# Kernel optimization log

Hardware: AMD Instinct MI355X
Metric: run time of the kernel (lower is better)

## Reference

```python
import jax, jax.numpy as jnp
import numpy as np

B, N, D = 4, 2048, 256
ALPHA = 0.2  # LeakyReLU negative slope
NEG = -1e9


def setup_inputs() -> dict:
    key = jax.random.key(0)
    ks = jax.random.split(key, 16)
    f = lambda k, s: jax.random.normal(k, s, dtype=jnp.float32)
    sc = 0.02
    spk = jax.random.randint(ks[13], (B, N), 0, 2)
    intra_mask = (spk[:, :, None] == spk[:, None, :]).astype(jnp.int32)
    inter_mask = 1 - intra_mask
    return {
        'inp': f(ks[0], (B, N, D)),
        'emo_vector': f(ks[1], (B, N, D)),
        'event_csk_before': f(ks[2], (B, N, D)),
        'event_csk_after': f(ks[3], (B, N, D)),
        'emo_intra_csk': f(ks[4], (B, N, D)),
        'emo_inter_csk': f(ks[5], (B, N, D)),
        'int_intra_csk': f(ks[6], (B, N, D)),
        'int_inter_csk': f(ks[7], (B, N, D)),
        'W': f(ks[8], (D, D)) * sc,
        'a': f(ks[9], (2 * D,)) * sc,
        'csk_W': f(ks[10], (D, D)) * sc,
        'csk_b': jnp.zeros((D,), jnp.float32),
        'emo_lin_W': f(ks[11], (4, D, D)) * sc,  # order: weight, query, key, value
        'emo_lin_b': jnp.zeros((4, D), jnp.float32),
        'act_lin_W': f(ks[12], (4, D, D)) * sc,
        'act_lin_b': jnp.zeros((4, D), jnp.float32),
        'conv_len': jax.random.randint(ks[14], (B,), N // 2, N + 1),
        'intra_mask': intra_mask,
        'inter_mask': inter_mask,
    }


def _csk_measure(tv, hv, temo, icsk, ocsk, tim, tom, lin_W, lin_b, add_emo):
    # tv/temo: [B,1,D] target vectors; hv: [B,N,D]; tim/tom: [B,1,N] float masks
    wW, qW, kW, vW = lin_W
    wb, qb, kb, vb = lin_b
    q = (tv + temo if add_emo else tv) @ qW + qb            # [B,1,D]
    w_i = icsk @ wW + wb
    w_o = ocsk @ wW + wb
    k_base = hv @ kW + kb
    v_base = hv @ vW + vb
    k_i, v_i = k_base + w_i, v_base + w_i                   # [B,N,D]
    k_o, v_o = k_base + w_o, v_base + w_o
    inv = 1.0 / jnp.sqrt(jnp.float32(D))
    s_i = jnp.einsum('bqd,bnd->bqn', q, k_i) * inv * tim    # [B,1,N]
    s_o = jnp.einsum('bqd,bnd->bqn', q, k_o) * inv * tom
    m = tim + tom
    probs = jax.nn.softmax(jnp.where(m == 0, NEG, s_i + s_o), axis=-1)  # [B,1,N]
    p_i = (probs * tim).transpose(0, 2, 1)                  # [B,N,1]
    p_o = (probs * tom).transpose(0, 2, 1)
    target_enh = p_i * q + p_o * q                          # q broadcasts [B,1,D]->[B,N,D]
    csk_enh = p_i * v_i + p_o * v_o
    return target_enh + csk_enh, probs


def reference(inp, emo_vector, event_csk_before, event_csk_after,
              emo_intra_csk, emo_inter_csk, int_intra_csk, int_inter_csk,
              W, a, csk_W, csk_b, emo_lin_W, emo_lin_b, act_lin_W, act_lin_b,
              conv_len, intra_mask, inter_mask):
    im = intra_mask.astype(jnp.float32)
    om = inter_mask.astype(jnp.float32)
    h = inp @ W                                             # [B,N,D]
    evt = (event_csk_after @ csk_W + csk_b) + (event_csk_before @ csk_W + csk_b)
    # GAT scoring without materializing [B,N,N,2D]:
    # e[b,i,j] = leaky_relu(h[b,i].a1 + (h+evt)[b,j].a2)
    a1, a2 = a[:D], a[D:]
    s1 = h @ a1                                             # [B,N]
    s2 = (h + evt) @ a2                                     # [B,N]
    e_pair = jax.nn.leaky_relu(s1[:, :, None] + s2[:, None, :], ALPHA)  # [B,N,N]
    e = e_pair * im + e_pair * om
    adj = im + om
    attention = jax.nn.softmax(jnp.where(adj == 0, NEG, e), axis=-1)
    h_prime = jnp.einsum('bij,bjd->bid', attention, h)      # [B,N,D]
    # gather target (last utterance) per conversation
    b_idx = jnp.arange(inp.shape[0])
    t_idx = conv_len - 1
    tv = inp[b_idx, t_idx][:, None, :]                      # [B,1,D]
    temo = emo_vector[b_idx, t_idx][:, None, :]
    tim = im[b_idx, t_idx][:, None, :]                      # [B,1,N]
    tom = om[b_idx, t_idx][:, None, :]
    emo_conn, emo_probs = _csk_measure(tv, h_prime, temo, emo_intra_csk,
                                       emo_inter_csk, tim, tom,
                                       emo_lin_W, emo_lin_b, add_emo=True)
    int_conn, act_probs = _csk_measure(tv, h_prime, temo, int_intra_csk,
                                       int_inter_csk, tim, tom,
                                       act_lin_W, act_lin_b, add_emo=False)
    out = h_prime + inp + emo_conn + int_conn
    return jax.nn.relu(out), emo_probs, act_probs
```

## Files before the change

kernel.cpp:

```cpp
#include <hip/hip_runtime.h>
#include <math.h>


namespace {
constexpr int B = 4, N = 2048, D = 256;
constexpr float ALPHA = 0.2f;
constexpr float INVS  = 0.0625f;

constexpr size_t OFF_H     = 0;
constexpr size_t OFF_HP    = 2097152;
constexpr size_t OFF_UE    = 4194304;
constexpr size_t OFF_UA    = 6291456;
constexpr size_t OFF_PPOS  = 8388608;
constexpr size_t OFF_PNEG  = 10486784;
constexpr size_t OFF_VE    = OFF_PPOS;
constexpr size_t OFF_VA    = OFF_PNEG;
constexpr size_t OFF_S1    = 12584960;
constexpr size_t OFF_S2    = OFF_S1 + 8192;
constexpr size_t OFF_SV    = OFF_S2 + 8192;
constexpr size_t OFF_SIDX  = OFF_SV + 8192;
constexpr size_t OFF_WP    = OFF_SIDX + 8192;
constexpr size_t OFF_WN    = OFF_WP + 8192;
constexpr size_t OFF_ZP    = OFF_WN + 8192;
constexpr size_t OFF_ZN    = OFF_ZP + 8196;
constexpr size_t OFF_PARTP = OFF_ZN + 8196;
constexpr size_t OFF_PARTN = OFF_PARTP + 32768;
constexpr size_t OFF_LE    = OFF_PARTN + 32768;
constexpr size_t OFF_LA    = OFF_LE + 8192;
constexpr size_t OFF_SET   = OFF_LA + 8192;
constexpr size_t KQE = OFF_SET + 0;
constexpr size_t WQE = OFF_SET + 1024;
constexpr size_t KQA = OFF_SET + 2048;
constexpr size_t WQA = OFF_SET + 3072;
constexpr size_t QCE = OFF_SET + 4096;
constexpr size_t QCA = OFF_SET + 5120;
constexpr size_t CA2 = OFF_SET + 6144;
constexpr size_t CEc = OFF_SET + 6400;
constexpr size_t CAc = OFF_SET + 6404;
constexpr size_t C2c = OFF_SET + 6408;
constexpr size_t OFF_RNK   = OFF_SET + 8192;
constexpr size_t OFF_C0    = OFF_RNK + 8192;
constexpr size_t OFF_C1    = OFF_C0 + 8192;
constexpr size_t OFF_PARTQ = OFF_C1 + 8192;
constexpr size_t OFF_QE    = OFF_PARTQ + 32768;
constexpr size_t OFF_QA    = OFF_QE + 1024;
constexpr size_t OFF_BT    = OFF_QA + 1024;
constexpr size_t OFF_PCNT  = OFF_BT + 163840;
}

typedef __attribute__((ext_vector_type(8))) short bf16x8;
typedef __attribute__((ext_vector_type(4))) float f32x4;

__device__ inline float wave_sum(float v) {
#pragma unroll
  for (int off = 32; off > 0; off >>= 1) v += __shfl_xor(v, off, 64);
  return v;
}

__device__ inline ushort f2bf(float x) {
  union { float f; uint u; } v; v.f = x;
  return (ushort)((v.u + 0x7FFFu + ((v.u >> 16) & 1u)) >> 16);
}
__device__ inline uint pk2bf(float a, float b) {
  return (uint)f2bf(a) | ((uint)f2bf(b) << 16);
}

__global__ __launch_bounds__(256) void k_bt(
    const float* __restrict__ Wm, const float* __restrict__ eW,
    const float* __restrict__ aW, ushort* __restrict__ bt)
{
  int m = blockIdx.y;
  const float* src = (m == 0) ? Wm : (m == 1) ? eW + 3*65536 : (m == 2) ? eW
                   : (m == 3) ? aW + 3*65536 : aW;
  ushort* dst = bt + (size_t)m*65536;
  int k0 = (blockIdx.x >> 2)*64, n0 = (blockIdx.x & 3)*64;
  __shared__ float tile[64][65];
  int r = threadIdx.x >> 2, c0 = (threadIdx.x & 3)*16;
#pragma unroll
  for (int cc = 0; cc < 16; cc += 4)
    *(float4*)&tile[r][c0+cc] = *(const float4*)&src[(size_t)(k0+r)*256 + n0 + c0 + cc];
  __syncthreads();
  int n = threadIdx.x >> 2, kq = (threadIdx.x & 3)*16;
  uint4 o0, o1;
  o0.x = pk2bf(tile[kq+ 0][n], tile[kq+ 1][n]);
  o0.y = pk2bf(tile[kq+ 2][n], tile[kq+ 3][n]);
  o0.z = pk2bf(tile[kq+ 4][n], tile[kq+ 5][n]);
  o0.w = pk2bf(tile[kq+ 6][n], tile[kq+ 7][n]);
  o1.x = pk2bf(tile[kq+ 8][n], tile[kq+ 9][n]);
  o1.y = pk2bf(tile[kq+10][n], tile[kq+11][n]);
  o1.z = pk2bf(tile[kq+12][n], tile[kq+13][n]);
  o1.w = pk2bf(tile[kq+14][n], tile[kq+15][n]);
  *(uint4*)&dst[(size_t)(n0+n)*256 + k0 + kq]     = o0;
  *(uint4*)&dst[(size_t)(n0+n)*256 + k0 + kq + 8] = o1;
}

__device__ __forceinline__ void mgemm_body(ushort* As,
    const float* __restrict__ A1, const ushort* __restrict__ B1,
    const float* __restrict__ A2, const ushort* __restrict__ B2,
    float* __restrict__ C)
{
  const int t = threadIdx.x;
  const int lane = t & 63, w = t >> 6;
  const int wm = w >> 1, wn = w & 1;
  const int laneN = lane & 15, kg = lane >> 4;
  const int m0 = blockIdx.x * 64, n0 = blockIdx.y * 128;
  const int srow = t >> 2, sq = t & 3;
  f32x4 acc[2][4] = {};
  for (int src = 0; src < 2; ++src) {
    const float* A = src ? A2 : A1;
    const ushort* Bt = src ? B2 : B1;
    if (!A) break;
    for (int k0 = 0; k0 < 256; k0 += 32) {
      __syncthreads();
      float4 f0 = *(const float4*)&A[(size_t)(m0 + srow)*256 + k0 + sq*8];
      float4 f1 = *(const float4*)&A[(size_t)(m0 + srow)*256 + k0 + sq*8 + 4];
      uint4 o;
      o.x = pk2bf(f0.x, f0.y); o.y = pk2bf(f0.z, f0.w);
      o.z = pk2bf(f1.x, f1.y); o.w = pk2bf(f1.z, f1.w);
      *(uint4*)&As[srow*40 + sq*8] = o;
      __syncthreads();
      bf16x8 bf[4];
#pragma unroll
      for (int j = 0; j < 4; ++j)
        bf[j] = *(const bf16x8*)&Bt[(size_t)(n0 + wn*64 + j*16 + laneN)*256 + k0 + kg*8];
#pragma unroll
      for (int i = 0; i < 2; ++i) {
        bf16x8 af = *(const bf16x8*)&As[(wm*32 + i*16 + laneN)*40 + kg*8];
#pragma unroll
        for (int j = 0; j < 4; ++j)
          acc[i][j] = __builtin_amdgcn_mfma_f32_16x16x32_bf16(af, bf[j], acc[i][j], 0, 0, 0);
      }
    }
  }
#pragma unroll
  for (int i = 0; i < 2; ++i)
#pragma unroll
    for (int j = 0; j < 4; ++j)
#pragma unroll
      for (int r = 0; r < 4; ++r)
        C[(size_t)(m0 + wm*32 + i*16 + kg*4 + r)*256 + n0 + wn*64 + j*16 + laneN]
            = acc[i][j][r];
}

__global__ __launch_bounds__(256) void k_mgemmh(
    const float* __restrict__ A1, const ushort* __restrict__ bt,
    float* __restrict__ C)
{
  __shared__ ushort As[64*40];
  mgemm_body(As, A1, bt, nullptr, nullptr, C);
}

__global__ __launch_bounds__(256) void k_mgemm2(
    const float* __restrict__ hp, const ushort* __restrict__ bt,
    float* __restrict__ ws)
{
  __shared__ ushort As[64*40];
  int z = blockIdx.z;
  const float* A2 = ws + (z ? OFF_UA : OFF_UE);
  const ushort* B1 = bt + (size_t)(z ? 3 : 1)*65536;
  const ushort* B2 = bt + (size_t)(z ? 4 : 2)*65536;
  float* C = ws + (z ? OFF_VA : OFF_VE);
  mgemm_body(As, hp, B1, A2, B2, C);
}

__global__ __launch_bounds__(256) void k_qpart(
    const float* __restrict__ inp, const float* __restrict__ emo,
    const float* __restrict__ eW, const float* __restrict__ aW,
    const int* __restrict__ cl, float* __restrict__ ws)
{
  int c = blockIdx.x;
  int m = blockIdx.y;
  int d = threadIdx.x;
  __shared__ float xs[B][16];
  if (d < 64) {
    int b = d >> 4, kk = d & 15;
    int t = cl[b] - 1;
    size_t idx = ((size_t)b*N + t)*D + c*16 + kk;
    float v = inp[idx];
    if (m == 0) v += emo[idx];
    xs[b][kk] = v;
  }
  __syncthreads();
  const float* Wq = (m ? aW : eW) + (size_t)D*D;
  float acc0 = 0.f, acc1 = 0.f, acc2 = 0.f, acc3 = 0.f;
#pragma unroll
  for (int kk = 0; kk < 16; ++kk) {
    int k = c*16 + kk;
    float w = Wq[(size_t)k*D + d];
    acc0 += xs[0][kk]*w; acc1 += xs[1][kk]*w;
    acc2 += xs[2][kk]*w; acc3 += xs[3][kk]*w;
  }
  size_t base = OFF_PARTQ + ((size_t)(m*16 + c)*4)*256 + d;
  ws[base + 0*256] = acc0; ws[base + 1*256] = acc1;
  ws[base + 2*256] = acc2; ws[base + 3*256] = acc3;
}

__global__ __launch_bounds__(256) void k_qfinish(
    const float* __restrict__ eb, const float* __restrict__ ab,
    const float* __restrict__ cskb, const float* __restrict__ a,
    float* __restrict__ ws)
{
  int b = blockIdx.x, m = blockIdx.y, d = threadIdx.x;
  __shared__ float red[D];
  const float* bias = m ? ab : eb;
  float q = bias[D + d];
#pragma unroll
  for (int c = 0; c < 16; ++c)
    q += ws[OFF_PARTQ + ((size_t)(m*16 + c)*4 + b)*256 + d];
  ws[(m ? OFF_QA : OFF_QE) + (size_t)b*D + d] = q;
  ws[(m ? QCA : QCE) + (size_t)b*D + d] = q + bias[3*D + d] + bias[0*D + d];
  red[d] = q * (bias[2*D + d] + bias[0*D + d]);
  __syncthreads();
  for (int s = 128; s > 0; s >>= 1) { if (d < s) red[d] += red[d+s]; __syncthreads(); }
  if (d == 0) ws[(m ? CAc : CEc) + b] = red[0];
  if (m == 1 && b == 0) {
    __syncthreads();
    red[d] = cskb[d] * a[D + d];
    __syncthreads();
    for (int s = 128; s > 0; s >>= 1) { if (d < s) red[d] += red[d+s]; __syncthreads(); }
    if (d == 0) ws[C2c] = 2.0f * red[0];
  }
}

__global__ __launch_bounds__(256) void k_rowdots(
    const float* __restrict__ eW, const float* __restrict__ aW,
    const float* __restrict__ cskW, const float* __restrict__ a,
    float* __restrict__ ws)
{
  int job = blockIdx.y;
  int wid = threadIdx.x >> 6, lane = threadIdx.x & 63;
  int row = blockIdx.x*4 + wid;
  __shared__ float vec[D];
  const float* M; size_t outo;
  if (job < 16) {
    int b = job >> 2, m = (job >> 1) & 1, which = job & 1;
    const float* base = m ? aW : eW;
    M = base + (which ? 0 : (size_t)2*D*D);
    if (threadIdx.x < D)
      vec[threadIdx.x] = ws[(m ? OFF_QA : OFF_QE) + (size_t)b*D + threadIdx.x];
    outo = (which ? (m ? WQA : WQE) : (m ? KQA : KQE)) + (size_t)b*D;
  } else {
    M = cskW;
    if (threadIdx.x < D) vec[threadIdx.x] = a[D + threadIdx.x];
    outo = CA2;
  }
  __syncthreads();
  float4 w = *reinterpret_cast<const float4*>(&M[(size_t)row*D + lane*4]);
  float s = w.x*vec[lane*4] + w.y*vec[lane*4+1] + w.z*vec[lane*4+2] + w.w*vec[lane*4+3];
  s = wave_sum(s);
  if (lane == 0) ws[outo + row] = s;
}

__global__ __launch_bounds__(256) void k_u(
    const float* __restrict__ ei, const float* __restrict__ eo,
    const float* __restrict__ ai, const float* __restrict__ ao,
    const int* __restrict__ cl, const int* __restrict__ intra,
    float* __restrict__ ws)
{
  size_t g = (size_t)blockIdx.x*256 + threadIdx.x;
  size_t base = g << 2;
  int b = (int)(base >> 19);
  int n = (int)((base >> 8) & (N - 1));
  int t = cl[b] - 1;
  float tm = (float)intra[(size_t)b*N*N + (size_t)t*N + n];
  float om = 1.0f - tm;
  float4 vei = *(const float4*)&ei[base];
  float4 veo = *(const float4*)&eo[base];
  float4 vai = *(const float4*)&ai[base];
  float4 vao = *(const float4*)&ao[base];
  float4 ue, ua;
  ue.x = tm*vei.x + om*veo.x; ue.y = tm*vei.y + om*veo.y;
  ue.z = tm*vei.z + om*veo.z; ue.w = tm*vei.w + om*veo.w;
  ua.x = tm*vai.x + om*vao.x; ua.y = tm*vai.y + om*vao.y;
  ua.z = tm*vai.z + om*vao.z; ua.w = tm*vai.w + om*vao.w;
  *(float4*)&ws[OFF_UE + base] = ue;
  *(float4*)&ws[OFF_UA + base] = ua;
}

__global__ __launch_bounds__(256) void k_s12(
    const float* __restrict__ bef, const float* __restrict__ aft,
    const float* __restrict__ a, float* __restrict__ ws)
{
  int wid  = (int)(((size_t)blockIdx.x*256 + threadIdx.x) >> 6);
  int lane = threadIdx.x & 63;
  int d0 = lane << 2;
  float4 a1 = *(const float4*)&a[d0];
  float4 a2 = *(const float4*)&a[D + d0];
  float4 cv = *(const float4*)&ws[CA2 + d0];
  float c2  = ws[C2c];
  for (int rr = 0; rr < 4; ++rr) {
    int row = wid*4 + rr;
    float4 h4 = *(const float4*)&ws[OFF_H + (size_t)row*D + d0];
    float4 b4 = *(const float4*)&bef[(size_t)row*D + d0];
    float4 f4 = *(const float4*)&aft[(size_t)row*D + d0];
    float s1 = h4.x*a1.x + h4.y*a1.y + h4.z*a1.z + h4.w*a1.w;
    float s2 = h4.x*a2.x + h4.y*a2.y + h4.z*a2.z + h4.w*a2.w
             + (b4.x+f4.x)*cv.x + (b4.y+f4.y)*cv.y
             + (b4.z+f4.z)*cv.z + (b4.w+f4.w)*cv.w;
    s1 = wave_sum(s1); s2 = wave_sum(s2);
    if (lane == 0) { ws[OFF_S1 + row] = s1; ws[OFF_S2 + row] = s2 + c2; }
  }
}

__global__ __launch_bounds__(256) void k_cnt2(float* __restrict__ ws)
{
  int jb = blockIdx.x;
  int kb = blockIdx.y;
  int b  = blockIdx.z;
  int tid = threadIdx.x;
  __shared__ float ck[128];
  if (tid < 32)
    *(float4*)&ck[tid*4] = *(const float4*)&ws[OFF_S2 + (size_t)b*N + kb*128 + tid*4];
  __syncthreads();
  int j = jb*256 + tid;
  float v = ws[OFF_S2 + (size_t)b*N + j];
  int kg = kb*128;
  int cnt = 0;
#pragma unroll
  for (int k = 0; k < 128; k += 16) {
    float4 u0 = *(const float4*)&ck[k];
    float4 u1 = *(const float4*)&ck[k+4];
    float4 u2 = *(const float4*)&ck[k+8];
    float4 u3 = *(const float4*)&ck[k+12];
    cnt += (u0.x < v) || (u0.x == v && (kg+k+ 0) < j);
    cnt += (u0.y < v) || (u0.y == v && (kg+k+ 1) < j);
    cnt += (u0.z < v) || (u0.z == v && (kg+k+ 2) < j);
    cnt += (u0.w < v) || (u0.w == v && (kg+k+ 3) < j);
    cnt += (u1.x < v) || (u1.x == v && (kg+k+ 4) < j);
    cnt += (u1.y < v) || (u1.y == v && (kg+k+ 5) < j);
    cnt += (u1.z < v) || (u1.z == v && (kg+k+ 6) < j);
    cnt += (u1.w < v) || (u1.w == v && (kg+k+ 7) < j);
    cnt += (u2.x < v) || (u2.x == v && (kg+k+ 8) < j);
    cnt += (u2.y < v) || (u2.y == v && (kg+k+ 9) < j);
    cnt += (u2.z < v) || (u2.z == v && (kg+k+10) < j);
    cnt += (u2.w < v) || (u2.w == v && (kg+k+11) < j);
    cnt += (u3.x < v) || (u3.x == v && (kg+k+12) < j);
    cnt += (u3.y < v) || (u3.y == v && (kg+k+13) < j);
    cnt += (u3.z < v) || (u3.z == v && (kg+k+14) < j);
    cnt += (u3.w < v) || (u3.w == v && (kg+k+15) < j);
  }
  ((int*)ws)[OFF_PCNT + ((size_t)(b*16 + kb))*N + j] = cnt;
}

__global__ __launch_bounds__(256) void k_cntfin(float* __restrict__ ws)
{
  int b = blockIdx.y;
  int j = blockIdx.x*256 + threadIdx.x;
  int cnt = 0;
#pragma unroll
  for (int kb = 0; kb < 16; ++kb)
    cnt += ((const int*)ws)[OFF_PCNT + ((size_t)(b*16 + kb))*N + j];
  float v = ws[OFF_S2 + (size_t)b*N + j];
  size_t o = (size_t)b*N + cnt;
  ws[OFF_SV + o] = v;
  ((int*)ws)[OFF_SIDX + o] = j;
  ws[OFF_WP + o] = expf(v);
  ws[OFF_WN + o] = expf(ALPHA*v);
}

__global__ __launch_bounds__(1024) void k_scan(float* __restrict__ ws)
{
  int b = blockIdx.x, m = blockIdx.y, t = threadIdx.x;
  const float* src = ws + (m ? OFF_WN : OFF_WP) + (size_t)b*N;
  float* dst = ws + (m ? OFF_ZN : OFF_ZP) + (size_t)b*(N+1);
  __shared__ float buf[N];
  buf[t] = src[t]; buf[t + 1024] = src[t + 1024];
  __syncthreads();
  for (int off = 1; off < N; off <<= 1) {
    float v0 = (t >= off)        ? buf[t - off]        : 0.f;
    float v1 = (t + 1024 >= off) ? buf[t + 1024 - off] : 0.f;
    __syncthreads();
    buf[t] += v0; buf[t + 1024] += v1;
    __syncthreads();
  }
  if (t == 0) dst[0] = 0.f;
  dst[t + 1]    = buf[t];
  dst[t + 1025] = buf[t + 1024];
}

__global__ __launch_bounds__(256) void k_rank(float* __restrict__ ws)
{
  int b = blockIdx.y;
  int i = blockIdx.x * 256 + threadIdx.x;
  __shared__ float sv[N];
  for (int r = threadIdx.x; r < N; r += 256) sv[r] = ws[OFF_SV + (size_t)b*N + r];
  __syncthreads();
  float s1i = ws[OFF_S1 + (size_t)b*N + i];
  float th = -s1i;
  int lo = 0, hi = N;
  while (lo < hi) { int mid = (lo + hi) >> 1; if (sv[mid] <= th) lo = mid + 1; else hi = mid; }
  int r = lo;
  float ep = expf(s1i), en = expf(ALPHA*s1i);
  float zp  = ws[OFF_ZP + (size_t)b*(N+1) + r];
  float zn  = ws[OFF_ZN + (size_t)b*(N+1) + r];
  float zpT = ws[OFF_ZP + (size_t)b*(N+1) + N];
  float den = ep*(zpT - zp) + en*zn;
  ((int*)ws)[OFF_RNK + (size_t)b*N + i] = r;
  ws[OFF_C0 + (size_t)b*N + i] = ep/den;
  ws[OFF_C1 + (size_t)b*N + i] = en/den;
}

__global__ __launch_bounds__(256) void k_p1(float* __restrict__ ws)
{
  int c = blockIdx.x, b = blockIdx.y, d = threadIdx.x;
  const int*   sidx = (const int*)ws + OFF_SIDX + (size_t)b*N;
  const float* wp = ws + OFF_WP + (size_t)b*N;
  const float* wn = ws + OFF_WN + (size_t)b*N;
  const float* h  = ws + OFF_H + (size_t)b*N*D;
  float ap = 0.f, an = 0.f;
  for (int r = c*64; r < c*64 + 64; ++r) {
    float hv = h[(size_t)sidx[r]*D + d];
    ap += wp[r]*hv; an += wn[r]*hv;
  }
  ws[OFF_PARTP + ((size_t)b*32 + c)*D + d] = ap;
  ws[OFF_PARTN + ((size_t)b*32 + c)*D + d] = an;
}

__global__ __launch_bounds__(256) void k_p3(float* __restrict__ ws)
{
  int c = blockIdx.x, b = blockIdx.y, d = threadIdx.x;
  const int*   sidx = (const int*)ws + OFF_SIDX + (size_t)b*N;
  const float* wp = ws + OFF_WP + (size_t)b*N;
  const float* wn = ws + OFF_WN + (size_t)b*N;
  const float* h  = ws + OFF_H + (size_t)b*N*D;
  float ap = 0.f, an = 0.f;
  for (int c2 = 0; c2 < c; ++c2) {
    ap += ws[OFF_PARTP + ((size_t)b*32 + c2)*D + d];
    an += ws[OFF_PARTN + ((size_t)b*32 + c2)*D + d];
  }
  for (int r = c*64; r < c*64 + 64; ++r) {
    ws[OFF_PPOS + ((size_t)b*(N+1) + r)*D + d] = ap;
    ws[OFF_PNEG + ((size_t)b*(N+1) + r)*D + d] = an;
    float hv = h[(size_t)sidx[r]*D + d];
    ap += wp[r]*hv; an += wn[r]*hv;
  }
  if (c == 31) {
    ws[OFF_PPOS + ((size_t)b*(N+1) + N)*D + d] = ap;
    ws[OFF_PNEG + ((size_t)b*(N+1) + N)*D + d] = an;
  }
}

__global__ __launch_bounds__(256) void k_hprime2(float* __restrict__ ws)
{
  int b = blockIdx.y, d = threadIdx.x;
  int i0 = blockIdx.x * 8;
  float totp = ws[OFF_PPOS + ((size_t)b*(N+1) + N)*D + d];
  float kqe = ws[KQE + (size_t)b*D + d], wqe = ws[WQE + (size_t)b*D + d];
  float kqa = ws[KQA + (size_t)b*D + d], wqa = ws[WQA + (size_t)b*D + d];
  float se[8], sa[8];
#pragma unroll
  for (int ii = 0; ii < 8; ++ii) {
    int i = i0 + ii;
    int   r  = ((const int*)ws)[OFF_RNK + (size_t)b*N + i];
    float c0 = ws[OFF_C0 + (size_t)b*N + i];
    float c1 = ws[OFF_C1 + (size_t)b*N + i];
    float pp = ws[OFF_PPOS + ((size_t)b*(N+1) + r)*D + d];
    float pn = ws[OFF_PNEG + ((size_t)b*(N+1) + r)*D + d];
    float v = c0*(totp - pp) + c1*pn;
    size_t base = ((size_t)b*N + i)*D + d;
    ws[OFF_HP + base] = v;
    float ue = ws[OFF_UE + base], ua = ws[OFF_UA + base];
    se[ii] = v*kqe + ue*wqe;
    sa[ii] = v*kqa + ua*wqa;
  }
  __shared__ float lred[16][4];
  int w = d >> 6, lane = d & 63;
#pragma unroll
  for (int ii = 0; ii < 8; ++ii) {
    float s = wave_sum(se[ii]);
    if (lane == 0) lred[ii][w] = s;
    s = wave_sum(sa[ii]);
    if (lane == 0) lred[8 + ii][w] = s;
  }
  __syncthreads();
  if (d < 16) {
    float s = lred[d][0] + lred[d][1] + lred[d][2] + lred[d][3];
    size_t row = (size_t)b*N + i0 + (d & 7);
    if (d < 8) ws[OFF_LE + row] = (s + ws[CEc + b]) * INVS;
    else       ws[OFF_LA + row] = (s + ws[CAc + b]) * INVS;
  }
}

__global__ __launch_bounds__(1024) void k_softmax(const float* __restrict__ ws,
                                                  float* __restrict__ out)
{
  int b = blockIdx.x, t = threadIdx.x;
  __shared__ float red[1024];
  for (int m = 0; m < 2; ++m) {
    const float* l = ws + (m ? OFF_LA : OFF_LE) + (size_t)b*N;
    float* p = out + (size_t)B*N*D + (size_t)m*B*N + (size_t)b*N;
    float v0 = l[t], v1 = l[t + 1024];
    red[t] = fmaxf(v0, v1);
    __syncthreads();
    for (int s = 512; s > 0; s >>= 1) { if (t < s) red[t] = fmaxf(red[t], red[t+s]); __syncthreads(); }
    float mx = red[0];
    __syncthreads();
    float e0 = expf(v0 - mx), e1 = expf(v1 - mx);
    red[t] = e0 + e1;
    __syncthreads();
    for (int s = 512; s > 0; s >>= 1) { if (t < s) red[t] += red[t+s]; __syncthreads(); }
    float inv = 1.0f / red[0];
    __syncthreads();
    p[t] = e0 * inv; p[t + 1024] = e1 * inv;
    __syncthreads();
  }
}

__global__ __launch_bounds__(256) void k_final(
    const float* __restrict__ inp, const float* __restrict__ ws,
    float* __restrict__ out)
{
  size_t g = (size_t)blockIdx.x*256 + threadIdx.x;
  size_t base = g << 2;
  int b  = (int)(base >> 19);
  int n  = (int)((base >> 8) & (N - 1));
  int d0 = (int)(base & (D - 1));
  float pe = out[(size_t)B*N*D + (size_t)b*N + n];
  float pa = out[(size_t)B*N*D + (size_t)B*N + (size_t)b*N + n];
  float4 hp = *(const float4*)&ws[OFF_HP + base];
  float4 iv = *(const float4*)&inp[base];
  float4 ve = *(const float4*)&ws[OFF_VE + base];
  float4 va = *(const float4*)&ws[OFF_VA + base];
  float4 qe = *(const float4*)&ws[QCE + (size_t)b*D + d0];
  float4 qa = *(const float4*)&ws[QCA + (size_t)b*D + d0];
  float4 o;
  o.x = hp.x + iv.x + pe*(qe.x + ve.x) + pa*(qa.x + va.x);
  o.y = hp.y + iv.y + pe*(qe.y + ve.y) + pa*(qa.y + va.y);
  o.z = hp.z + iv.z + pe*(qe.z + ve.z) + pa*(qa.z + va.z);
  o.w = hp.w + iv.w + pe*(qe.w + ve.w) + pa*(qa.w + va.w);
  o.x = fmaxf(o.x, 0.f); o.y = fmaxf(o.y, 0.f);
  o.z = fmaxf(o.z, 0.f); o.w = fmaxf(o.w, 0.f);
  *(float4*)&out[base] = o;
}

extern "C" void kernel_launch(void* const* d_in, const int* in_sizes, int n_in,
                              void* d_out, int out_size, void* d_ws, size_t ws_size,
                              hipStream_t stream) {
  const float* inp  = (const float*)d_in[0];
  const float* emo  = (const float*)d_in[1];
  const float* bef  = (const float*)d_in[2];
  const float* aft  = (const float*)d_in[3];
  const float* ei   = (const float*)d_in[4];
  const float* eo   = (const float*)d_in[5];
  const float* ii   = (const float*)d_in[6];
  const float* io   = (const float*)d_in[7];
  const float* W    = (const float*)d_in[8];
  const float* a    = (const float*)d_in[9];
  const float* cskW = (const float*)d_in[10];
  const float* cskb = (const float*)d_in[11];
  const float* eW   = (const float*)d_in[12];
  const float* eb   = (const float*)d_in[13];
  const float* aW   = (const float*)d_in[14];
  const float* ab   = (const float*)d_in[15];
  const int*   cl   = (const int*)d_in[16];
  const int*   intra= (const int*)d_in[17];
  float* ws  = (float*)d_ws;
  float* out = (float*)d_out;
  ushort* bt = (ushort*)(ws + OFF_BT);

  k_bt<<<dim3(16, 5), 256, 0, stream>>>(W, eW, aW, bt);
  k_qpart<<<dim3(16, 2), 256, 0, stream>>>(inp, emo, eW, aW, cl, ws);
  k_mgemmh<<<dim3(128, 2), 256, 0, stream>>>(inp, bt, ws + OFF_H);
  k_qfinish<<<dim3(B, 2), 256, 0, stream>>>(eb, ab, cskb, a, ws);
  k_u<<<2048, 256, 0, stream>>>(ei, eo, ii, io, cl, intra, ws);
  k_rowdots<<<dim3(64, 17), 256, 0, stream>>>(eW, aW, cskW, a, ws);
  k_s12<<<512, 256, 0, stream>>>(bef, aft, a, ws);
  k_cnt2<<<dim3(8, 16, B), 256, 0, stream>>>(ws);
  k_cntfin<<<dim3(8, B), 256, 0, stream>>>(ws);
  k_scan<<<dim3(B, 2), 1024, 0, stream>>>(ws);
  k_rank<<<dim3(8, B), 256, 0, stream>>>(ws);
  k_p1<<<dim3(32, B), 256, 0, stream>>>(ws);
  k_p3<<<dim3(32, B), 256, 0, stream>>>(ws);
  k_hprime2<<<dim3(256, B), 256, 0, stream>>>(ws);
  k_mgemm2<<<dim3(128, 2, 2), 256, 0, stream>>>(ws + OFF_HP, bt, ws);
  k_softmax<<<B, 1024, 0, stream>>>(ws, out);
  k_final<<<2048, 256, 0, stream>>>(inp, ws, out);
}
```

Baseline: 140.0 us.

## Fuse value GEMM with softmax apply and final epilogue; merge setup kernels

Merges the weight transpose and query-partial kernels into one launch. It moves the u·wq dot products into k_u so k_hprime2 no longer rereads the U buffers. The softmax is split into a small stats reduction, and the exp normalisation plus final residual/ReLU output is fused into a new combined value GEMM. That GEMM computes both emo and act projections in one block, which removes the VE/VA intermediate buffers and two launches. It relies on k_rowdots now running before k_u so WQE/WQA are ready, and the new GEMM uses smaller 32-row tiles across 256 blocks.

```diff
diff --git a/kernel.cpp b/kernel.cpp
--- a/kernel.cpp
+++ b/kernel.cpp
@@ -13,8 +13,6 @@
 constexpr size_t OFF_UA    = 6291456;
 constexpr size_t OFF_PPOS  = 8388608;
 constexpr size_t OFF_PNEG  = 10486784;
-constexpr size_t OFF_VE    = OFF_PPOS;
-constexpr size_t OFF_VA    = OFF_PNEG;
 constexpr size_t OFF_S1    = 12584960;
 constexpr size_t OFF_S2    = OFF_S1 + 8192;
 constexpr size_t OFF_SV    = OFF_S2 + 8192;
@@ -46,6 +44,12 @@
 constexpr size_t OFF_QA    = OFF_QE + 1024;
 constexpr size_t OFF_BT    = OFF_QA + 1024;
 constexpr size_t OFF_PCNT  = OFF_BT + 163840;
+constexpr size_t OFF_LEU   = OFF_PCNT + 131072;
+constexpr size_t OFF_LAU   = OFF_LEU + 8192;
+constexpr size_t SMXE      = OFF_LAU + 8192;
+constexpr size_t SIVE      = SMXE + 4;
+constexpr size_t SMXA      = SIVE + 4;
+constexpr size_t SIVA      = SMXA + 4;
 }
 
 typedef __attribute__((ext_vector_type(8))) short bf16x8;
@@ -65,40 +69,69 @@
   return (uint)f2bf(a) | ((uint)f2bf(b) << 16);
 }
 
-__global__ __launch_bounds__(256) void k_bt(
+__global__ __launch_bounds__(256) void k_btq(
     const float* __restrict__ Wm, const float* __restrict__ eW,
-    const float* __restrict__ aW, ushort* __restrict__ bt)
-{
-  int m = blockIdx.y;
-  const float* src = (m == 0) ? Wm : (m == 1) ? eW + 3*65536 : (m == 2) ? eW
-                   : (m == 3) ? aW + 3*65536 : aW;
-  ushort* dst = bt + (size_t)m*65536;
-  int k0 = (blockIdx.x >> 2)*64, n0 = (blockIdx.x & 3)*64;
-  __shared__ float tile[64][65];
-  int r = threadIdx.x >> 2, c0 = (threadIdx.x & 3)*16;
-#pragma unroll
-  for (int cc = 0; cc < 16; cc += 4)
-    *(float4*)&tile[r][c0+cc] = *(const float4*)&src[(size_t)(k0+r)*256 + n0 + c0 + cc];
-  __syncthreads();
-  int n = threadIdx.x >> 2, kq = (threadIdx.x & 3)*16;
-  uint4 o0, o1;
-  o0.x = pk2bf(tile[kq+ 0][n], tile[kq+ 1][n]);
-  o0.y = pk2bf(tile[kq+ 2][n], tile[kq+ 3][n]);
-  o0.z = pk2bf(tile[kq+ 4][n], tile[kq+ 5][n]);
-  o0.w = pk2bf(tile[kq+ 6][n], tile[kq+ 7][n]);
-  o1.x = pk2bf(tile[kq+ 8][n], tile[kq+ 9][n]);
-  o1.y = pk2bf(tile[kq+10][n], tile[kq+11][n]);
-  o1.z = pk2bf(tile[kq+12][n], tile[kq+13][n]);
-  o1.w = pk2bf(tile[kq+14][n], tile[kq+15][n]);
-  *(uint4*)&dst[(size_t)(n0+n)*256 + k0 + kq]     = o0;
-  *(uint4*)&dst[(size_t)(n0+n)*256 + k0 + kq + 8] = o1;
-}
-
-__device__ __forceinline__ void mgemm_body(ushort* As,
-    const float* __restrict__ A1, const ushort* __restrict__ B1,
-    const float* __restrict__ A2, const ushort* __restrict__ B2,
+    const float* __restrict__ aW, const float* __restrict__ inp,
+    const float* __restrict__ emo, const int* __restrict__ cl,
+    ushort* __restrict__ bt, float* __restrict__ ws)
+{
+  __shared__ float smem[64*65];
+  if (blockIdx.y < 5) {
+    int m = blockIdx.y;
+    const float* src = (m == 0) ? Wm : (m == 1) ? eW + 3*65536 : (m == 2) ? eW
+                     : (m == 3) ? aW + 3*65536 : aW;
+    ushort* dst = bt + (size_t)m*65536;
+    int k0 = (blockIdx.x >> 2)*64, n0 = (blockIdx.x & 3)*64;
+    int r = threadIdx.x >> 2, c0 = (threadIdx.x & 3)*16;
+#pragma unroll
+    for (int cc = 0; cc < 16; cc += 4)
+      *(float4*)&smem[r*65 + c0+cc] = *(const float4*)&src[(size_t)(k0+r)*256 + n0 + c0 + cc];
+    __syncthreads();
+    int n = threadIdx.x >> 2, kq = (threadIdx.x & 3)*16;
+    uint4 o0, o1;
+    o0.x = pk2bf(smem[(kq+ 0)*65+n], smem[(kq+ 1)*65+n]);
+    o0.y = pk2bf(smem[(kq+ 2)*65+n], smem[(kq+ 3)*65+n]);
+    o0.z = pk2bf(smem[(kq+ 4)*65+n], smem[(kq+ 5)*65+n]);
+    o0.w = pk2bf(smem[(kq+ 6)*65+n], smem[(kq+ 7)*65+n]);
+    o1.x = pk2bf(smem[(kq+ 8)*65+n], smem[(kq+ 9)*65+n]);
+    o1.y = pk2bf(smem[(kq+10)*65+n], smem[(kq+11)*65+n]);
+    o1.z = pk2bf(smem[(kq+12)*65+n], smem[(kq+13)*65+n]);
+    o1.w = pk2bf(smem[(kq+14)*65+n], smem[(kq+15)*65+n]);
+    *(uint4*)&dst[(size_t)(n0+n)*256 + k0 + kq]     = o0;
+    *(uint4*)&dst[(size_t)(n0+n)*256 + k0 + kq + 8] = o1;
+  } else {
+    int c = blockIdx.x;
+    int m = blockIdx.y - 5;
+    int d = threadIdx.x;
+    if (d < 64) {
+      int b = d >> 4, kk = d & 15;
+      int t = cl[b] - 1;
+      size_t idx = ((size_t)b*N + t)*D + c*16 + kk;
+      float v = inp[idx];
+      if (m == 0) v += emo[idx];
+      smem[b*16 + kk] = v;
+    }
+    __syncthreads();
+    const float* Wq = (m ? aW : eW) + (size_t)D*D;
+    float acc0 = 0.f, acc1 = 0.f, acc2 = 0.f, acc3 = 0.f;
+#pragma unroll
+    for (int kk = 0; kk < 16; ++kk) {
+      int k = c*16 + kk;
+      float w = Wq[(size_t)k*D + d];
+      acc0 += smem[0*16+kk]*w; acc1 += smem[1*16+kk]*w;
+      acc2 += smem[2*16+kk]*w; acc3 += smem[3*16+kk]*w;
+    }
+    size_t base = OFF_PARTQ + ((size_t)(m*16 + c)*4)*256 + d;
+    ws[base + 0*256] = acc0; ws[base + 1*256] = acc1;
+    ws[base + 2*256] = acc2; ws[base + 3*256] = acc3;
+  }
+}
+
+__global__ __launch_bounds__(256) void k_mgemmh(
+    const float* __restrict__ A1, const ushort* __restrict__ bt,
     float* __restrict__ C)
 {
+  __shared__ ushort As[64*40];
   const int t = threadIdx.x;
   const int lane = t & 63, w = t >> 6;
   const int wm = w >> 1, wn = w & 1;
@@ -106,30 +139,25 @@
   const int m0 = blockIdx.x * 64, n0 = blockIdx.y * 128;
   const int srow = t >> 2, sq = t & 3;
   f32x4 acc[2][4] = {};
-  for (int src = 0; src < 2; ++src) {
-    const float* A = src ? A2 : A1;
-    const ushort* Bt = src ? B2 : B1;
-    if (!A) break;
-    for (int k0 = 0; k0 < 256; k0 += 32) {
-      __syncthreads();
-      float4 f0 = *(const float4*)&A[(size_t)(m0 + srow)*256 + k0 + sq*8];
-      float4 f1 = *(const float4*)&A[(size_t)(m0 + srow)*256 + k0 + sq*8 + 4];
-      uint4 o;
-      o.x = pk2bf(f0.x, f0.y); o.y = pk2bf(f0.z, f0.w);
-      o.z = pk2bf(f1.x, f1.y); o.w = pk2bf(f1.z, f1.w);
-      *(uint4*)&As[srow*40 + sq*8] = o;
-      __syncthreads();
-      bf16x8 bf[4];
+  for (int k0 = 0; k0 < 256; k0 += 32) {
+    __syncthreads();
+    float4 f0 = *(const float4*)&A1[(size_t)(m0 + srow)*256 + k0 + sq*8];
+    float4 f1 = *(const float4*)&A1[(size_t)(m0 + srow)*256 + k0 + sq*8 + 4];
+    uint4 o;
+    o.x = pk2bf(f0.x, f0.y); o.y = pk2bf(f0.z, f0.w);
+    o.z = pk2bf(f1.x, f1.y); o.w = pk2bf(f1.z, f1.w);
+    *(uint4*)&As[srow*40 + sq*8] = o;
+    __syncthreads();
+    bf16x8 bf[4];
+#pragma unroll
+    for (int j = 0; j < 4; ++j)
+      bf[j] = *(const bf16x8*)&bt[(size_t)(n0 + wn*64 + j*16 + laneN)*256 + k0 + kg*8];
+#pragma unroll
+    for (int i = 0; i < 2; ++i) {
+      bf16x8 af = *(const bf16x8*)&As[(wm*32 + i*16 + laneN)*40 + kg*8];
 #pragma unroll
       for (int j = 0; j < 4; ++j)
-        bf[j] = *(const bf16x8*)&Bt[(size_t)(n0 + wn*64 + j*16 + laneN)*256 + k0 + kg*8];
-#pragma unroll
-      for (int i = 0; i < 2; ++i) {
-        bf16x8 af = *(const bf16x8*)&As[(wm*32 + i*16 + laneN)*40 + kg*8];
-#pragma unroll
-        for (int j = 0; j < 4; ++j)
-          acc[i][j] = __builtin_amdgcn_mfma_f32_16x16x32_bf16(af, bf[j], acc[i][j], 0, 0, 0);
-      }
+        acc[i][j] = __builtin_amdgcn_mfma_f32_16x16x32_bf16(af, bf[j], acc[i][j], 0, 0, 0);
     }
   }
 #pragma unroll
@@ -140,59 +168,6 @@
       for (int r = 0; r < 4; ++r)
         C[(size_t)(m0 + wm*32 + i*16 + kg*4 + r)*256 + n0 + wn*64 + j*16 + laneN]
             = acc[i][j][r];
-}
-
-__global__ __launch_bounds__(256) void k_mgemmh(
-    const float* __restrict__ A1, const ushort* __restrict__ bt,
-    float* __restrict__ C)
-{
-  __shared__ ushort As[64*40];
-  mgemm_body(As, A1, bt, nullptr, nullptr, C);
-}
-
-__global__ __launch_bounds__(256) void k_mgemm2(
-    const float* __restrict__ hp, const ushort* __restrict__ bt,
-    float* __restrict__ ws)
-{
-  __shared__ ushort As[64*40];
-  int z = blockIdx.z;
-  const float* A2 = ws + (z ? OFF_UA : OFF_UE);
-  const ushort* B1 = bt + (size_t)(z ? 3 : 1)*65536;
-  const ushort* B2 = bt + (size_t)(z ? 4 : 2)*65536;
-  float* C = ws + (z ? OFF_VA : OFF_VE);
-  mgemm_body(As, hp, B1, A2, B2, C);
-}
-
-__global__ __launch_bounds__(256) void k_qpart(
-    const float* __restrict__ inp, const float* __restrict__ emo,
-    const float* __restrict__ eW, const float* __restrict__ aW,
-    const int* __restrict__ cl, float* __restrict__ ws)
-{
-  int c = blockIdx.x;
-  int m = blockIdx.y;
-  int d = threadIdx.x;
-  __shared__ float xs[B][16];
-  if (d < 64) {
-    int b = d >> 4, kk = d & 15;
-    int t = cl[b] - 1;
-    size_t idx = ((size_t)b*N + t)*D + c*16 + kk;
-    float v = inp[idx];
-    if (m == 0) v += emo[idx];
-    xs[b][kk] = v;
-  }
-  __syncthreads();
-  const float* Wq = (m ? aW : eW) + (size_t)D*D;
-  float acc0 = 0.f, acc1 = 0.f, acc2 = 0.f, acc3 = 0.f;
-#pragma unroll
-  for (int kk = 0; kk < 16; ++kk) {
-    int k = c*16 + kk;
-    float w = Wq[(size_t)k*D + d];
-    acc0 += xs[0][kk]*w; acc1 += xs[1][kk]*w;
-    acc2 += xs[2][kk]*w; acc3 += xs[3][kk]*w;
-  }
-  size_t base = OFF_PARTQ + ((size_t)(m*16 + c)*4)*256 + d;
-  ws[base + 0*256] = acc0; ws[base + 1*256] = acc1;
-  ws[base + 2*256] = acc2; ws[base + 3*256] = acc3;
 }
 
 __global__ __launch_bounds__(256) void k_qfinish(
@@ -261,6 +236,7 @@
   size_t base = g << 2;
   int b = (int)(base >> 19);
   int n = (int)((base >> 8) & (N - 1));
+  int d0 = (int)(base & (D - 1));
   int t = cl[b] - 1;
   float tm = (float)intra[(size_t)b*N*N + (size_t)t*N + n];
   float om = 1.0f - tm;
@@ -275,6 +251,16 @@
   ua.z = tm*vai.z + om*vao.z; ua.w = tm*vai.w + om*vao.w;
   *(float4*)&ws[OFF_UE + base] = ue;
   *(float4*)&ws[OFF_UA + base] = ua;
+  float4 wqe = *(const float4*)&ws[WQE + (size_t)b*D + d0];
+  float4 wqa = *(const float4*)&ws[WQA + (size_t)b*D + d0];
+  float se = ue.x*wqe.x + ue.y*wqe.y + ue.z*wqe.z + ue.w*wqe.w;
+  float sa = ua.x*wqa.x + ua.y*wqa.y + ua.z*wqa.z + ua.w*wqa.w;
+  se = wave_sum(se); sa = wave_sum(sa);
+  if ((threadIdx.x & 63) == 0) {
+    size_t row = base >> 8;
+    ws[OFF_LEU + row] = se;
+    ws[OFF_LAU + row] = sa;
+  }
 }
 
 __global__ __launch_bounds__(256) void k_s12(
@@ -445,8 +431,8 @@
   int b = blockIdx.y, d = threadIdx.x;
   int i0 = blockIdx.x * 8;
   float totp = ws[OFF_PPOS + ((size_t)b*(N+1) + N)*D + d];
-  float kqe = ws[KQE + (size_t)b*D + d], wqe = ws[WQE + (size_t)b*D + d];
-  float kqa = ws[KQA + (size_t)b*D + d], wqa = ws[WQA + (size_t)b*D + d];
+  float kqe = ws[KQE + (size_t)b*D + d];
+  float kqa = ws[KQA + (size_t)b*D + d];
   float se[8], sa[8];
 #pragma unroll
   for (int ii = 0; ii < 8; ++ii) {
@@ -457,11 +443,9 @@
     float pp = ws[OFF_PPOS + ((size_t)b*(N+1) + r)*D + d];
     float pn = ws[OFF_PNEG + ((size_t)b*(N+1) + r)*D + d];
     float v = c0*(totp - pp) + c1*pn;
-    size_t base = ((size_t)b*N + i)*D + d;
-    ws[OFF_HP + base] = v;
-    float ue = ws[OFF_UE + base], ua = ws[OFF_UA + base];
-    se[ii] = v*kqe + ue*wqe;
-    sa[ii] = v*kqa + ua*wqa;
+    ws[OFF_HP + ((size_t)b*N + i)*D + d] = v;
+    se[ii] = v*kqe;
+    sa[ii] = v*kqa;
   }
   __shared__ float lred[16][4];
   int w = d >> 6, lane = d & 63;
@@ -476,61 +460,106 @@
   if (d < 16) {
     float s = lred[d][0] + lred[d][1] + lred[d][2] + lred[d][3];
     size_t row = (size_t)b*N + i0 + (d & 7);
-    if (d < 8) ws[OFF_LE + row] = (s + ws[CEc + b]) * INVS;
-    else       ws[OFF_LA + row] = (s + ws[CAc + b]) * INVS;
-  }
-}
-
-__global__ __launch_bounds__(1024) void k_softmax(const float* __restrict__ ws,
-                                                  float* __restrict__ out)
-{
-  int b = blockIdx.x, t = threadIdx.x;
-  __shared__ float red[1024];
-  for (int m = 0; m < 2; ++m) {
-    const float* l = ws + (m ? OFF_LA : OFF_LE) + (size_t)b*N;
-    float* p = out + (size_t)B*N*D + (size_t)m*B*N + (size_t)b*N;
-    float v0 = l[t], v1 = l[t + 1024];
-    red[t] = fmaxf(v0, v1);
-    __syncthreads();
-    for (int s = 512; s > 0; s >>= 1) { if (t < s) red[t] = fmaxf(red[t], red[t+s]); __syncthreads(); }
-    float mx = red[0];
-    __syncthreads();
-    float e0 = expf(v0 - mx), e1 = expf(v1 - mx);
-    red[t] = e0 + e1;
-    __syncthreads();
-    for (int s = 512; s > 0; s >>= 1) { if (t < s) red[t] += red[t+s]; __syncthreads(); }
-    float inv = 1.0f / red[0];
-    __syncthreads();
-    p[t] = e0 * inv; p[t + 1024] = e1 * inv;
-    __syncthreads();
-  }
-}
-
-__global__ __launch_bounds__(256) void k_final(
-    const float* __restrict__ inp, const float* __restrict__ ws,
-    float* __restrict__ out)
-{
-  size_t g = (size_t)blockIdx.x*256 + threadIdx.x;
-  size_t base = g << 2;
-  int b  = (int)(base >> 19);
-  int n  = (int)((base >> 8) & (N - 1));
-  int d0 = (int)(base & (D - 1));
-  float pe = out[(size_t)B*N*D + (size_t)b*N + n];
-  float pa = out[(size_t)B*N*D + (size_t)B*N + (size_t)b*N + n];
-  float4 hp = *(const float4*)&ws[OFF_HP + base];
-  float4 iv = *(const float4*)&inp[base];
-  float4 ve = *(const float4*)&ws[OFF_VE + base];
-  float4 va = *(const float4*)&ws[OFF_VA + base];
-  float4 qe = *(const float4*)&ws[QCE + (size_t)b*D + d0];
-  float4 qa = *(const float4*)&ws[QCA + (size_t)b*D + d0];
-  float4 o;
-  o.x = hp.x + iv.x + pe*(qe.x + ve.x) + pa*(qa.x + va.x);
-  o.y = hp.y + iv.y + pe*(qe.y + ve.y) + pa*(qa.y + va.y);
-  o.z = hp.z + iv.z + pe*(qe.z + ve.z) + pa*(qa.z + va.z);
-  o.w = hp.w + iv.w + pe*(qe.w + ve.w) + pa*(qa.w + va.w);
-  o.x = fmaxf(o.x, 0.f); o.y = fmaxf(o.y, 0.f);
-  o.z = fmaxf(o.z, 0.f); o.w = fmaxf(o.w, 0.f);
-  *(float4*)&out[base] = o;
+    if (d < 8) ws[OFF_LE + row] = (s + ws[OFF_LEU + row] + ws[CEc + b]) * INVS;
+    else       ws[OFF_LA + row] = (s + ws[OFF_LAU + row] + ws[CAc + b]) * INVS;
+  }
+}
+
+__global__ __launch_bounds__(256) void k_smred(float* __restrict__ ws)
+{
+  int b = blockIdx.x, m = blockIdx.y, t = threadIdx.x;
+  const float* l = ws + (m ? OFF_LA : OFF_LE) + (size_t)b*N;
+  __shared__ float red[256];
+  float v[8];
+  float mx = -1e30f;
+#pragma unroll
+  for (int k = 0; k < 8; ++k) { v[k] = l[t*8 + k]; mx = fmaxf(mx, v[k]); }
+  red[t] = mx; __syncthreads();
+  for (int s = 128; s > 0; s >>= 1) { if (t < s) red[t] = fmaxf(red[t], red[t+s]); __syncthreads(); }
+  mx = red[0]; __syncthreads();
+  float sum = 0.f;
+#pragma unroll
+  for (int k = 0; k < 8; ++k) sum += expf(v[k] - mx);
+  red[t] = sum; __syncthreads();
+  for (int s = 128; s > 0; s >>= 1) { if (t < s) red[t] += red[t+s]; __syncthreads(); }
+  if (t == 0) {
+    ws[(m ? SMXA : SMXE) + b] = mx;
+    ws[(m ? SIVA : SIVE) + b] = 1.0f / red[0];
+  }
+}
+
+__global__ __launch_bounds__(512) void k_mgemm2f(
+    const float* __restrict__ inp, const ushort* __restrict__ bt,
+    float* __restrict__ ws, float* __restrict__ out)
+{
+  __shared__ ushort Hs[32*40], Es[32*40], Zs[32*40];
+  __shared__ float qec[256], qac[256];
+  const int t = threadIdx.x;
+  const int m0 = blockIdx.x * 32;
+  const int b = m0 >> 11;
+  const int lane = t & 63, w = t >> 6;
+  const int wm = w >> 2, wn = w & 3;
+  const int laneN = lane & 15, kg = lane >> 4;
+  if (t < 256) qec[t] = ws[QCE + (size_t)b*D + t];
+  else         qac[t - 256] = ws[QCA + (size_t)b*D + (t - 256)];
+  const int srow = t >> 4, so = (t & 15) * 2;
+  const float* hp = ws + OFF_HP;
+  const float* ue = ws + OFF_UE;
+  const float* ua = ws + OFF_UA;
+  const ushort* Bve = bt + 1*65536;
+  const ushort* Bwe = bt + 2*65536;
+  const ushort* Bva = bt + 3*65536;
+  const ushort* Bwa = bt + 4*65536;
+  f32x4 accE[4] = {}, accA[4] = {};
+  for (int k0 = 0; k0 < 256; k0 += 32) {
+    __syncthreads();
+    size_t abase = (size_t)(m0 + srow)*256 + k0 + so;
+    float2 h2 = *(const float2*)&hp[abase];
+    float2 e2 = *(const float2*)&ue[abase];
+    float2 z2 = *(const float2*)&ua[abase];
+    *(uint*)&Hs[srow*40 + so] = pk2bf(h2.x, h2.y);
+    *(uint*)&Es[srow*40 + so] = pk2bf(e2.x, e2.y);
+    *(uint*)&Zs[srow*40 + so] = pk2bf(z2.x, z2.y);
+    __syncthreads();
+    bf16x8 hf = *(const bf16x8*)&Hs[(wm*16 + laneN)*40 + kg*8];
+    bf16x8 ef = *(const bf16x8*)&Es[(wm*16 + laneN)*40 + kg*8];
+    bf16x8 zf = *(const bf16x8*)&Zs[(wm*16 + laneN)*40 + kg*8];
+#pragma unroll
+    for (int j = 0; j < 4; ++j) {
+      size_t cb = (size_t)(wn*64 + j*16 + laneN)*256 + k0 + kg*8;
+      bf16x8 bve = *(const bf16x8*)&Bve[cb];
+      bf16x8 bwe = *(const bf16x8*)&Bwe[cb];
+      bf16x8 bva = *(const bf16x8*)&Bva[cb];
+      bf16x8 bwa = *(const bf16x8*)&Bwa[cb];
+      accE[j] = __builtin_amdgcn_mfma_f32_16x16x32_bf16(hf, bve, accE[j], 0, 0, 0);
+      accE[j] = __builtin_amdgcn_mfma_f32_16x16x32_bf16(ef, bwe, accE[j], 0, 0, 0);
+      accA[j] = __builtin_amdgcn_mfma_f32_16x16x32_bf16(hf, bva, accA[j], 0, 0, 0);
+      accA[j] = __builtin_amdgcn_mfma_f32_16x16x32_bf16(zf, bwa, accA[j], 0, 0, 0);
+    }
+  }
+  float smxe = ws[SMXE + b], sive = ws[SIVE + b];
+  float smxa = ws[SMXA + b], siva = ws[SIVA + b];
+  if (t < 32) {
+    size_t row = (size_t)m0 + t;
+    int n = (int)(row & (N - 1));
+    float pe = expf(ws[OFF_LE + row] - smxe) * sive;
+    float pa = expf(ws[OFF_LA + row] - smxa) * siva;
+    out[(size_t)B*N*D + (size_t)b*N + n] = pe;
+    out[(size_t)B*N*D + (size_t)B*N + (size_t)b*N + n] = pa;
+  }
+#pragma unroll
+  for (int r = 0; r < 4; ++r) {
+    size_t row = (size_t)m0 + wm*16 + kg*4 + r;
+    float pe = expf(ws[OFF_LE + row] - smxe) * sive;
+    float pa = expf(ws[OFF_LA + row] - smxa) * siva;
+#pragma unroll
+    for (int j = 0; j < 4; ++j) {
+      int col = wn*64 + j*16 + laneN;
+      size_t idx = row*256 + col;
+      float o = hp[idx] + inp[idx] + pe*(qec[col] + accE[j][r]) + pa*(qac[col] + accA[j][r]);
+      out[idx] = fmaxf(o, 0.f);
+    }
+  }
 }
 
 extern "C" void kernel_launch(void* const* d_in, const int* in_sizes, int n_in,
@@ -558,12 +587,11 @@
   float* out = (float*)d_out;
   ushort* bt = (ushort*)(ws + OFF_BT);
 
-  k_bt<<<dim3(16, 5), 256, 0, stream>>>(W, eW, aW, bt);
-  k_qpart<<<dim3(16, 2), 256, 0, stream>>>(inp, emo, eW, aW, cl, ws);
+  k_btq<<<dim3(16, 7), 256, 0, stream>>>(W, eW, aW, inp, emo, cl, bt, ws);
   k_mgemmh<<<dim3(128, 2), 256, 0, stream>>>(inp, bt, ws + OFF_H);
   k_qfinish<<<dim3(B, 2), 256, 0, stream>>>(eb, ab, cskb, a, ws);
+  k_rowdots<<<dim3(64, 17), 256, 0, stream>>>(eW, aW, cskW, a, ws);
   k_u<<<2048, 256, 0, stream>>>(ei, eo, ii, io, cl, intra, ws);
-  k_rowdots<<<dim3(64, 17), 256, 0, stream>>>(eW, aW, cskW, a, ws);
   k_s12<<<512, 256, 0, stream>>>(bef, aft, a, ws);
   k_cnt2<<<dim3(8, 16, B), 256, 0, stream>>>(ws);
   k_cntfin<<<dim3(8, B), 256, 0, stream>>>(ws);
@@ -572,7 +600,6 @@
   k_p1<<<dim3(32, B), 256, 0, stream>>>(ws);
   k_p3<<<dim3(32, B), 256, 0, stream>>>(ws);
   k_hprime2<<<dim3(256, B), 256, 0, stream>>>(ws);
-  k_mgemm2<<<dim3(128, 2, 2), 256, 0, stream>>>(ws + OFF_HP, bt, ws);
-  k_softmax<<<B, 1024, 0, stream>>>(ws, out);
-  k_final<<<2048, 256, 0, stream>>>(inp, ws, out);
-}
+  k_smred<<<dim3(B, 2), 256, 0, stream>>>(ws);
+  k_mgemm2f<<<256, 512, 0, stream>>>(inp, bt, ws, out);
+}
```

After: 142.2 us. About the same (+1.6%).
